# Performance work log

Hardware: AMD Instinct MI355X
Metric: run time of the kernel (lower is better)

The kernel has to match this reference:

```python
import jax, jax.numpy as jnp
import numpy as np

B, L, H, W, C = 2, 5, 48, 176, 256
HEADS, DIM_HEAD = 8, 32
INNER = HEADS * DIM_HEAD  # 256
SCALE = DIM_HEAD ** -0.5


def setup_inputs() -> dict:
    key = jax.random.key(0)
    k1, k2, k3, k4, k5 = jax.random.split(key, 5)
    x = jax.random.normal(k1, (B, L, H, W, C), dtype=jnp.float32)
    # mask of shape (B, H, W, 1, L); slot 0 always valid so no softmax row is fully masked
    mask = jax.random.randint(k2, (B, H, W, 1, L), 0, 2, dtype=jnp.int32)
    mask = mask.at[..., 0].set(1)
    w_qkv = jax.random.normal(k3, (C, 3 * INNER), dtype=jnp.float32) / np.sqrt(C)
    w_out = jax.random.normal(k4, (INNER, C), dtype=jnp.float32) / np.sqrt(INNER)
    b_out = jax.random.normal(k5, (C,), dtype=jnp.float32) * 0.01
    return {"x": x, "mask": mask, "w_qkv": w_qkv, "w_out": w_out, "b_out": b_out}


def reference(x, mask, w_qkv, w_out, b_out):
    # x: (B, L, H, W, C) -> (B, H, W, L, C)
    xp = jnp.transpose(x, (0, 2, 3, 1, 4))
    qkv = xp @ w_qkv  # (B, H, W, L, 3*INNER)
    q, k, v = jnp.split(qkv, 3, axis=-1)
    # split heads: (B, H, W, L, M, D)
    shp = (B, H, W, L, HEADS, DIM_HEAD)
    q = q.reshape(shp)
    k = k.reshape(shp)
    v = v.reshape(shp)
    # attention over the small CAV axis L
    att = jnp.einsum('bhwimd,bhwjmd->bmhwij', q, k) * SCALE  # (B,M,H,W,L,L)
    m = mask[:, None]  # (B,1,H,W,1,L) broadcasts over (B,M,H,W,i,j)
    att = jnp.where(m == 0, -jnp.inf, att)
    att = jax.nn.softmax(att, axis=-1)
    out = jnp.einsum('bmhwij,bhwjmd->bhwimd', att, v)  # (B,H,W,L,M,D)
    out = out.reshape(B, H, W, L, INNER)
    out = out @ w_out + b_out  # dropout is identity in eval
    return jnp.transpose(out, (0, 3, 1, 2, 4))  # (B, L, H, W, C)
```

## Files before the change

kernel.cpp:

```cpp
#include <hip/hip_runtime.h>


typedef __attribute__((ext_vector_type(8))) short short8;
typedef __attribute__((ext_vector_type(4))) float f32x4;

#define SCALE_F 0.17677669529663687f

static __device__ __forceinline__ float b2f(unsigned short u) {
    union { unsigned u; float f; } x; x.u = ((unsigned)u) << 16; return x.f;
}
static __device__ __forceinline__ unsigned short f2b(float f) {
    union { float f; unsigned u; } x; x.f = f;
    unsigned u = x.u;
    return (unsigned short)((u + 0x7FFFu + ((u >> 16) & 1u)) >> 16);
}

static __device__ __forceinline__ size_t row_to_xoff(int r) {
    int l = r % 5; int t = r / 5;
    int w = t % 176; t /= 176;
    int h = t % 48; int b = t / 48;
    return (size_t)(((b * 5 + l) * 48 + h) * 176 + w) * 256;
}

static __device__ __forceinline__ int lidx(int r, int c) {
    return r * 256 + ((((c >> 3) ^ (r & 7)) << 3) | (c & 7));
}

static __device__ __forceinline__ void barrier_lgkm() {
    __builtin_amdgcn_s_waitcnt(0xC07F);
    __builtin_amdgcn_s_barrier();
}

__global__ __launch_bounds__(256) void k_prep(const float* __restrict__ wq,
                                              const float* __restrict__ wo,
                                              unsigned short* __restrict__ wqt,
                                              unsigned short* __restrict__ wot) {
    __shared__ unsigned short tile[64 * 65];
    const int bb = blockIdx.x;
    const float* src; unsigned short* dst; int kt, nt, ncols;
    if (bb < 48) { kt = bb / 12; nt = bb % 12; src = wq; dst = wqt; ncols = 768; }
    else { int b2 = bb - 48; kt = b2 >> 2; nt = b2 & 3; src = wo; dst = wot; ncols = 256; }
    const int t = threadIdx.x;
#pragma unroll
    for (int p = 0; p < 4; ++p) {
        int u = p * 256 + t; int r = u >> 4, c4 = u & 15;
        float4 v = *(const float4*)&src[(size_t)(kt * 64 + r) * ncols + nt * 64 + c4 * 4];
        tile[r * 65 + c4 * 4 + 0] = f2b(v.x);
        tile[r * 65 + c4 * 4 + 1] = f2b(v.y);
        tile[r * 65 + c4 * 4 + 2] = f2b(v.z);
        tile[r * 65 + c4 * 4 + 3] = f2b(v.w);
    }
    __syncthreads();
#pragma unroll
    for (int p = 0; p < 2; ++p) {
        int u = p * 256 + t; int n = u >> 3, c8 = u & 7;
        short8 o;
#pragma unroll
        for (int j = 0; j < 8; ++j) o[j] = (short)tile[(c8 * 8 + j) * 65 + n];
        *(short8*)&dst[(nt * 64 + n) * 256 + kt * 64 + c8 * 8] = o;
    }
}

static __device__ __forceinline__ void cstore(const f32x4 (&acc)[5][2],
        unsigned short* __restrict__ Ds, int n0w, int lane) {
    const int ln = lane & 15, quad = lane >> 4;
#pragma unroll
    for (int m = 0; m < 5; ++m)
#pragma unroll
        for (int n = 0; n < 2; ++n)
#pragma unroll
            for (int rg = 0; rg < 4; ++rg)
                Ds[lidx(m * 16 + quad * 4 + rg, n0w + n * 16 + ln)] = f2b(acc[m][n][rg]);
}

__global__ __launch_bounds__(512, 2) void k_fused(const float* __restrict__ x,
                                                  const int* __restrict__ mask,
                                                  const unsigned short* __restrict__ wqt,
                                                  const unsigned short* __restrict__ wot,
                                                  const float* __restrict__ bo,
                                                  float* __restrict__ out) {
    __shared__ __align__(16) unsigned short xs[80 * 256];
    __shared__ __align__(16) unsigned short qs[80 * 256];
    __shared__ __align__(16) unsigned short kvs[80 * 256];

    const int tid = threadIdx.x;
    const int blk = blockIdx.x;
    const int rbase = blk * 80;
    const int lane = tid & 63, wv = tid >> 6;
    const int n0w = wv * 32;
    const int ln = lane & 15, quad = lane >> 4;

#pragma unroll
    for (int i = 0; i < 5; ++i) {
        int u = i * 512 + tid;
        int r = u >> 5, cb = u & 31;
        size_t xo = row_to_xoff(rbase + r) + cb * 8;
        float4 v0 = *(const float4*)(x + xo);
        float4 v1 = *(const float4*)(x + xo + 4);
        short8 o;
        o[0] = (short)f2b(v0.x); o[1] = (short)f2b(v0.y);
        o[2] = (short)f2b(v0.z); o[3] = (short)f2b(v0.w);
        o[4] = (short)f2b(v1.x); o[5] = (short)f2b(v1.y);
        o[6] = (short)f2b(v1.z); o[7] = (short)f2b(v1.w);
        *(short8*)&xs[lidx(r, cb * 8)] = o;
    }

    const int part = tid & 3, hh = (tid >> 2) & 7, g = tid >> 5;
    int mk[5];
#pragma unroll
    for (int j = 0; j < 5; ++j) mk[j] = mask[(blk * 16 + g) * 5 + j];

    const unsigned short* wq_l = wqt + (n0w + ln) * 256 + quad * 8;
    const unsigned short* wo_l = wot + (n0w + ln) * 256 + quad * 8;

    barrier_lgkm();

    f32x4 aq[5][2], ak[5][2], av[5][2];
#pragma unroll
    for (int m = 0; m < 5; ++m)
#pragma unroll
        for (int n = 0; n < 2; ++n) {
            aq[m][n] = (f32x4){0.f, 0.f, 0.f, 0.f};
            ak[m][n] = (f32x4){0.f, 0.f, 0.f, 0.f};
            av[m][n] = (f32x4){0.f, 0.f, 0.f, 0.f};
        }
#pragma unroll
    for (int kk = 0; kk < 8; ++kk) {
        short8 a[5];
#pragma unroll
        for (int m = 0; m < 5; ++m)
            a[m] = *(const short8*)&xs[lidx(m * 16 + ln, kk * 32 + quad * 8)];
        short8 bq[2], bk[2], bv[2];
#pragma unroll
        for (int n = 0; n < 2; ++n) {
            int o = n * (16 * 256) + kk * 32;
            bq[n] = *(const short8*)&wq_l[o];
            bk[n] = *(const short8*)&wq_l[o + 256 * 256];
            bv[n] = *(const short8*)&wq_l[o + 512 * 256];
        }
#pragma unroll
        for (int m = 0; m < 5; ++m)
#pragma unroll
            for (int n = 0; n < 2; ++n)
                aq[m][n] = __builtin_amdgcn_mfma_f32_16x16x32_bf16(a[m], bq[n], aq[m][n], 0, 0, 0);
#pragma unroll
        for (int m = 0; m < 5; ++m)
#pragma unroll
            for (int n = 0; n < 2; ++n)
                ak[m][n] = __builtin_amdgcn_mfma_f32_16x16x32_bf16(a[m], bk[n], ak[m][n], 0, 0, 0);
#pragma unroll
        for (int m = 0; m < 5; ++m)
#pragma unroll
            for (int n = 0; n < 2; ++n)
                av[m][n] = __builtin_amdgcn_mfma_f32_16x16x32_bf16(a[m], bv[n], av[m][n], 0, 0, 0);
    }
    cstore(aq, qs, n0w, lane);
    cstore(ak, kvs, n0w, lane);
    barrier_lgkm();

    float pr[5][5];
    {
        const int c0 = hh * 32 + part * 8;
        float qf[5][8];
#pragma unroll
        for (int i = 0; i < 5; ++i) {
            short8 qv = *(const short8*)&qs[lidx(g * 5 + i, c0)];
#pragma unroll
            for (int d = 0; d < 8; ++d) qf[i][d] = b2f((unsigned short)qv[d]);
        }
        float s[5][5];
#pragma unroll
        for (int j = 0; j < 5; ++j) {
            short8 kv = *(const short8*)&kvs[lidx(g * 5 + j, c0)];
            float kf[8];
#pragma unroll
            for (int d = 0; d < 8; ++d) kf[d] = b2f((unsigned short)kv[d]);
#pragma unroll
            for (int i = 0; i < 5; ++i) {
                float acc = 0.f;
#pragma unroll
                for (int d = 0; d < 8; ++d) acc += qf[i][d] * kf[d];
                s[i][j] = acc;
            }
        }
#pragma unroll
        for (int i = 0; i < 5; ++i)
#pragma unroll
            for (int j = 0; j < 5; ++j) {
                s[i][j] += __shfl_xor(s[i][j], 1, 64);
                s[i][j] += __shfl_xor(s[i][j], 2, 64);
            }
#pragma unroll
        for (int i = 0; i < 5; ++i) {
            float mx = -1e30f;
#pragma unroll
            for (int j = 0; j < 5; ++j) {
                s[i][j] = mk[j] ? s[i][j] * SCALE_F : -1e30f;
                mx = fmaxf(mx, s[i][j]);
            }
            float sum = 0.f;
#pragma unroll
            for (int j = 0; j < 5; ++j) { pr[i][j] = __expf(s[i][j] - mx); sum += pr[i][j]; }
            float inv = 1.f / sum;
#pragma unroll
            for (int j = 0; j < 5; ++j) pr[i][j] *= inv;
        }
    }
    barrier_lgkm();

    cstore(av, kvs, n0w, lane);
    barrier_lgkm();

    {
        const int c0 = hh * 32 + part * 8;
        float o[5][8];
#pragma unroll
        for (int i = 0; i < 5; ++i)
#pragma unroll
            for (int d = 0; d < 8; ++d) o[i][d] = 0.f;
#pragma unroll
        for (int j = 0; j < 5; ++j) {
            short8 vv = *(const short8*)&kvs[lidx(g * 5 + j, c0)];
            float vf[8];
#pragma unroll
            for (int d = 0; d < 8; ++d) vf[d] = b2f((unsigned short)vv[d]);
#pragma unroll
            for (int i = 0; i < 5; ++i)
#pragma unroll
                for (int d = 0; d < 8; ++d) o[i][d] += pr[i][j] * vf[d];
        }
#pragma unroll
        for (int i = 0; i < 5; ++i) {
            short8 ov;
#pragma unroll
            for (int d = 0; d < 8; ++d) ov[d] = (short)f2b(o[i][d]);
            *(short8*)&kvs[lidx(g * 5 + i, c0)] = ov;
        }
    }
    barrier_lgkm();

    {
        f32x4 ao[5][2];
#pragma unroll
        for (int m = 0; m < 5; ++m)
#pragma unroll
            for (int n = 0; n < 2; ++n) ao[m][n] = (f32x4){0.f, 0.f, 0.f, 0.f};
#pragma unroll
        for (int kk = 0; kk < 8; ++kk) {
            short8 a[5];
#pragma unroll
            for (int m = 0; m < 5; ++m)
                a[m] = *(const short8*)&kvs[lidx(m * 16 + ln, kk * 32 + quad * 8)];
            short8 bn[2];
#pragma unroll
            for (int n = 0; n < 2; ++n)
                bn[n] = *(const short8*)&wo_l[n * (16 * 256) + kk * 32];
#pragma unroll
            for (int m = 0; m < 5; ++m)
#pragma unroll
                for (int n = 0; n < 2; ++n)
                    ao[m][n] = __builtin_amdgcn_mfma_f32_16x16x32_bf16(a[m], bn[n], ao[m][n], 0, 0, 0);
        }
        float bv2[2];
#pragma unroll
        for (int n = 0; n < 2; ++n) bv2[n] = bo[n0w + n * 16 + ln];
#pragma unroll
        for (int m = 0; m < 5; ++m)
#pragma unroll
            for (int rg = 0; rg < 4; ++rg) {
                int row = m * 16 + quad * 4 + rg;
                size_t off = row_to_xoff(rbase + row);
#pragma unroll
                for (int n = 0; n < 2; ++n)
                    out[off + n0w + n * 16 + ln] = ao[m][n][rg] + bv2[n];
            }
    }
}

extern "C" void kernel_launch(void* const* d_in, const int* in_sizes, int n_in,
                              void* d_out, int out_size, void* d_ws, size_t ws_size,
                              hipStream_t stream) {
    const float* x   = (const float*)d_in[0];
    const int* mask  = (const int*)d_in[1];
    const float* wq  = (const float*)d_in[2];
    const float* wo  = (const float*)d_in[3];
    const float* bo  = (const float*)d_in[4];
    float* out = (float*)d_out;

    char* ws = (char*)d_ws;
    unsigned short* wqt = (unsigned short*)(ws);
    unsigned short* wot = (unsigned short*)(ws + 393216);

    hipLaunchKernelGGL(k_prep, dim3(64), dim3(256), 0, stream, wq, wo, wqt, wot);
    hipLaunchKernelGGL(k_fused, dim3(1056), dim3(512), 0, stream, x, mask, wqt, wot, bo, out);
}
```

Before: 267.8 us.

## Double block to 1024 threads with 16 output columns per wave

The fused block now launches 1024 threads (16 waves), and each wave computes one 16-column MFMA tile instead of two, which halves the accumulator register footprint per thread. The V projection is moved into a separate loop that overlaps with the Q/K stores, and only the first 512 threads run the scalar attention stage. This is meant to raise latency hiding and wave occupancy, but half the threads sit idle during attention. Barriers also now span 16 waves, and launch bounds of 1024 with 4 blocks per CU may force register spills.

New measurement: 273.5 us. +2.1%, slower.

```diff
diff --git a/kernel.cpp b/kernel.cpp
--- a/kernel.cpp
+++ b/kernel.cpp
@@ -61,24 +61,22 @@
     }
 }
 
-static __device__ __forceinline__ void cstore(const f32x4 (&acc)[5][2],
+static __device__ __forceinline__ void cstore1(const f32x4 (&acc)[5],
         unsigned short* __restrict__ Ds, int n0w, int lane) {
     const int ln = lane & 15, quad = lane >> 4;
 #pragma unroll
     for (int m = 0; m < 5; ++m)
 #pragma unroll
-        for (int n = 0; n < 2; ++n)
-#pragma unroll
-            for (int rg = 0; rg < 4; ++rg)
-                Ds[lidx(m * 16 + quad * 4 + rg, n0w + n * 16 + ln)] = f2b(acc[m][n][rg]);
-}
-
-__global__ __launch_bounds__(512, 2) void k_fused(const float* __restrict__ x,
-                                                  const int* __restrict__ mask,
-                                                  const unsigned short* __restrict__ wqt,
-                                                  const unsigned short* __restrict__ wot,
-                                                  const float* __restrict__ bo,
-                                                  float* __restrict__ out) {
+        for (int rg = 0; rg < 4; ++rg)
+            Ds[lidx(m * 16 + quad * 4 + rg, n0w + ln)] = f2b(acc[m][rg]);
+}
+
+__global__ __launch_bounds__(1024, 4) void k_fused(const float* __restrict__ x,
+                                                   const int* __restrict__ mask,
+                                                   const unsigned short* __restrict__ wqt,
+                                                   const unsigned short* __restrict__ wot,
+                                                   const float* __restrict__ bo,
+                                                   float* __restrict__ out) {
     __shared__ __align__(16) unsigned short xs[80 * 256];
     __shared__ __align__(16) unsigned short qs[80 * 256];
     __shared__ __align__(16) unsigned short kvs[80 * 256];
@@ -87,79 +85,80 @@
     const int blk = blockIdx.x;
     const int rbase = blk * 80;
     const int lane = tid & 63, wv = tid >> 6;
-    const int n0w = wv * 32;
+    const int n0w = wv * 16;
     const int ln = lane & 15, quad = lane >> 4;
 
 #pragma unroll
-    for (int i = 0; i < 5; ++i) {
-        int u = i * 512 + tid;
-        int r = u >> 5, cb = u & 31;
-        size_t xo = row_to_xoff(rbase + r) + cb * 8;
-        float4 v0 = *(const float4*)(x + xo);
-        float4 v1 = *(const float4*)(x + xo + 4);
-        short8 o;
-        o[0] = (short)f2b(v0.x); o[1] = (short)f2b(v0.y);
-        o[2] = (short)f2b(v0.z); o[3] = (short)f2b(v0.w);
-        o[4] = (short)f2b(v1.x); o[5] = (short)f2b(v1.y);
-        o[6] = (short)f2b(v1.z); o[7] = (short)f2b(v1.w);
-        *(short8*)&xs[lidx(r, cb * 8)] = o;
-    }
-
-    const int part = tid & 3, hh = (tid >> 2) & 7, g = tid >> 5;
+    for (int i = 0; i < 3; ++i) {
+        int u = i * 1024 + tid;
+        if (u < 2560) {
+            int r = u >> 5, cb = u & 31;
+            size_t xo = row_to_xoff(rbase + r) + cb * 8;
+            float4 v0 = *(const float4*)(x + xo);
+            float4 v1 = *(const float4*)(x + xo + 4);
+            short8 o;
+            o[0] = (short)f2b(v0.x); o[1] = (short)f2b(v0.y);
+            o[2] = (short)f2b(v0.z); o[3] = (short)f2b(v0.w);
+            o[4] = (short)f2b(v1.x); o[5] = (short)f2b(v1.y);
+            o[6] = (short)f2b(v1.z); o[7] = (short)f2b(v1.w);
+            *(short8*)&xs[lidx(r, cb * 8)] = o;
+        }
+    }
+
+    const bool act = tid < 512;
+    const int part = tid & 3, hh = (tid >> 2) & 7, g = (tid >> 5) & 15;
     int mk[5];
 #pragma unroll
-    for (int j = 0; j < 5; ++j) mk[j] = mask[(blk * 16 + g) * 5 + j];
+    for (int j = 0; j < 5; ++j) mk[j] = act ? mask[(blk * 16 + g) * 5 + j] : 1;
 
     const unsigned short* wq_l = wqt + (n0w + ln) * 256 + quad * 8;
     const unsigned short* wo_l = wot + (n0w + ln) * 256 + quad * 8;
 
     barrier_lgkm();
 
-    f32x4 aq[5][2], ak[5][2], av[5][2];
-#pragma unroll
-    for (int m = 0; m < 5; ++m)
-#pragma unroll
-        for (int n = 0; n < 2; ++n) {
-            aq[m][n] = (f32x4){0.f, 0.f, 0.f, 0.f};
-            ak[m][n] = (f32x4){0.f, 0.f, 0.f, 0.f};
-            av[m][n] = (f32x4){0.f, 0.f, 0.f, 0.f};
-        }
+    f32x4 aq[5], ak[5];
+#pragma unroll
+    for (int m = 0; m < 5; ++m) {
+        aq[m] = (f32x4){0.f, 0.f, 0.f, 0.f};
+        ak[m] = (f32x4){0.f, 0.f, 0.f, 0.f};
+    }
 #pragma unroll
     for (int kk = 0; kk < 8; ++kk) {
         short8 a[5];
 #pragma unroll
         for (int m = 0; m < 5; ++m)
             a[m] = *(const short8*)&xs[lidx(m * 16 + ln, kk * 32 + quad * 8)];
-        short8 bq[2], bk[2], bv[2];
-#pragma unroll
-        for (int n = 0; n < 2; ++n) {
-            int o = n * (16 * 256) + kk * 32;
-            bq[n] = *(const short8*)&wq_l[o];
-            bk[n] = *(const short8*)&wq_l[o + 256 * 256];
-            bv[n] = *(const short8*)&wq_l[o + 512 * 256];
-        }
-#pragma unroll
-        for (int m = 0; m < 5; ++m)
-#pragma unroll
-            for (int n = 0; n < 2; ++n)
-                aq[m][n] = __builtin_amdgcn_mfma_f32_16x16x32_bf16(a[m], bq[n], aq[m][n], 0, 0, 0);
-#pragma unroll
-        for (int m = 0; m < 5; ++m)
-#pragma unroll
-            for (int n = 0; n < 2; ++n)
-                ak[m][n] = __builtin_amdgcn_mfma_f32_16x16x32_bf16(a[m], bk[n], ak[m][n], 0, 0, 0);
-#pragma unroll
-        for (int m = 0; m < 5; ++m)
-#pragma unroll
-            for (int n = 0; n < 2; ++n)
-                av[m][n] = __builtin_amdgcn_mfma_f32_16x16x32_bf16(a[m], bv[n], av[m][n], 0, 0, 0);
-    }
-    cstore(aq, qs, n0w, lane);
-    cstore(ak, kvs, n0w, lane);
+        short8 bq = *(const short8*)&wq_l[kk * 32];
+        short8 bk = *(const short8*)&wq_l[65536 + kk * 32];
+#pragma unroll
+        for (int m = 0; m < 5; ++m)
+            aq[m] = __builtin_amdgcn_mfma_f32_16x16x32_bf16(a[m], bq, aq[m], 0, 0, 0);
+#pragma unroll
+        for (int m = 0; m < 5; ++m)
+            ak[m] = __builtin_amdgcn_mfma_f32_16x16x32_bf16(a[m], bk, ak[m], 0, 0, 0);
+    }
+    cstore1(aq, qs, n0w, lane);
+    cstore1(ak, kvs, n0w, lane);
+
+    f32x4 av[5];
+#pragma unroll
+    for (int m = 0; m < 5; ++m) av[m] = (f32x4){0.f, 0.f, 0.f, 0.f};
+#pragma unroll
+    for (int kk = 0; kk < 8; ++kk) {
+        short8 a[5];
+#pragma unroll
+        for (int m = 0; m < 5; ++m)
+            a[m] = *(const short8*)&xs[lidx(m * 16 + ln, kk * 32 + quad * 8)];
+        short8 bv = *(const short8*)&wq_l[131072 + kk * 32];
+#pragma unroll
+        for (int m = 0; m < 5; ++m)
+            av[m] = __builtin_amdgcn_mfma_f32_16x16x32_bf16(a[m], bv, av[m], 0, 0, 0);
+    }
+
     barrier_lgkm();
 
     float pr[5][5];
-    {
+    if (act) {
         const int c0 = hh * 32 + part * 8;
         float qf[5][8];
 #pragma unroll
@@ -208,10 +207,10 @@
     }
     barrier_lgkm();
 
-    cstore(av, kvs, n0w, lane);
-    barrier_lgkm();
-
-    {
+    cstore1(av, kvs, n0w, lane);
+    barrier_lgkm();
+
+    if (act) {
         const int c0 = hh * 32 + part * 8;
         float o[5][8];
 #pragma unroll
@@ -240,39 +239,28 @@
     barrier_lgkm();
 
     {
-        f32x4 ao[5][2];
-#pragma unroll
-        for (int m = 0; m < 5; ++m)
-#pragma unroll
-            for (int n = 0; n < 2; ++n) ao[m][n] = (f32x4){0.f, 0.f, 0.f, 0.f};
+        f32x4 ao[5];
+#pragma unroll
+        for (int m = 0; m < 5; ++m) ao[m] = (f32x4){0.f, 0.f, 0.f, 0.f};
 #pragma unroll
         for (int kk = 0; kk < 8; ++kk) {
             short8 a[5];
 #pragma unroll
             for (int m = 0; m < 5; ++m)
                 a[m] = *(const short8*)&kvs[lidx(m * 16 + ln, kk * 32 + quad * 8)];
-            short8 bn[2];
-#pragma unroll
-            for (int n = 0; n < 2; ++n)
-                bn[n] = *(const short8*)&wo_l[n * (16 * 256) + kk * 32];
+            short8 bn = *(const short8*)&wo_l[kk * 32];
 #pragma unroll
             for (int m = 0; m < 5; ++m)
-#pragma unroll
-                for (int n = 0; n < 2; ++n)
-                    ao[m][n] = __builtin_amdgcn_mfma_f32_16x16x32_bf16(a[m], bn[n], ao[m][n], 0, 0, 0);
-        }
-        float bv2[2];
-#pragma unroll
-        for (int n = 0; n < 2; ++n) bv2[n] = bo[n0w + n * 16 + ln];
+                ao[m] = __builtin_amdgcn_mfma_f32_16x16x32_bf16(a[m], bn, ao[m], 0, 0, 0);
+        }
+        float bv2 = bo[n0w + ln];
 #pragma unroll
         for (int m = 0; m < 5; ++m)
 #pragma unroll
             for (int rg = 0; rg < 4; ++rg) {
                 int row = m * 16 + quad * 4 + rg;
                 size_t off = row_to_xoff(rbase + row);
-#pragma unroll
-                for (int n = 0; n < 2; ++n)
-                    out[off + n0w + n * 16 + ln] = ao[m][n][rg] + bv2[n];
+                out[off + n0w + ln] = ao[m][rg] + bv2;
             }
     }
 }
@@ -292,5 +280,5 @@
     unsigned short* wot = (unsigned short*)(ws + 393216);
 
     hipLaunchKernelGGL(k_prep, dim3(64), dim3(256), 0, stream, wq, wo, wqt, wot);
-    hipLaunchKernelGGL(k_fused, dim3(1056), dim3(512), 0, stream, x, mask, wqt, wot, bo, out);
-}
+    hipLaunchKernelGGL(k_fused, dim3(1056), dim3(1024), 0, stream, x, mask, wqt, wot, bo, out);
+}
```

## Halve rows per block and split V projection to raise occupancy

Applied to the files above, without the earlier changes.

Each block now handles 40 rows (8 pixel groups) instead of 80, with shared buffers shrunk to 48 rows and the grid doubled to 2112 blocks. The V projection runs as a separate pass after Q/K are stored, which cuts the live accumulator count, and launch bounds ask for 4 blocks per CU. The aim is higher occupancy and better latency hiding. The cost is wasted MFMA work on padded rows 40-47, idle threads in the attention phase (only 256 of 512 active), and the x tile being read from LDS twice.

Measured after the change: 297.8 us. +11.2%, slower.

```diff
diff --git a/kernel.cpp b/kernel.cpp
--- a/kernel.cpp
+++ b/kernel.cpp
@@ -61,11 +61,11 @@
     }
 }
 
-static __device__ __forceinline__ void cstore(const f32x4 (&acc)[5][2],
+static __device__ __forceinline__ void cstore(const f32x4 (&acc)[3][2],
         unsigned short* __restrict__ Ds, int n0w, int lane) {
     const int ln = lane & 15, quad = lane >> 4;
 #pragma unroll
-    for (int m = 0; m < 5; ++m)
+    for (int m = 0; m < 3; ++m)
 #pragma unroll
         for (int n = 0; n < 2; ++n)
 #pragma unroll
@@ -73,93 +73,111 @@
                 Ds[lidx(m * 16 + quad * 4 + rg, n0w + n * 16 + ln)] = f2b(acc[m][n][rg]);
 }
 
-__global__ __launch_bounds__(512, 2) void k_fused(const float* __restrict__ x,
+__global__ __launch_bounds__(512, 4) void k_fused(const float* __restrict__ x,
                                                   const int* __restrict__ mask,
                                                   const unsigned short* __restrict__ wqt,
                                                   const unsigned short* __restrict__ wot,
                                                   const float* __restrict__ bo,
                                                   float* __restrict__ out) {
-    __shared__ __align__(16) unsigned short xs[80 * 256];
-    __shared__ __align__(16) unsigned short qs[80 * 256];
-    __shared__ __align__(16) unsigned short kvs[80 * 256];
+    __shared__ __align__(16) unsigned short xs[48 * 256];
+    __shared__ __align__(16) unsigned short qs[48 * 256];
+    __shared__ __align__(16) unsigned short kvs[48 * 256];
 
     const int tid = threadIdx.x;
     const int blk = blockIdx.x;
-    const int rbase = blk * 80;
+    const int rbase = blk * 40;
     const int lane = tid & 63, wv = tid >> 6;
     const int n0w = wv * 32;
     const int ln = lane & 15, quad = lane >> 4;
 
 #pragma unroll
-    for (int i = 0; i < 5; ++i) {
+    for (int i = 0; i < 3; ++i) {
         int u = i * 512 + tid;
-        int r = u >> 5, cb = u & 31;
-        size_t xo = row_to_xoff(rbase + r) + cb * 8;
-        float4 v0 = *(const float4*)(x + xo);
-        float4 v1 = *(const float4*)(x + xo + 4);
-        short8 o;
-        o[0] = (short)f2b(v0.x); o[1] = (short)f2b(v0.y);
-        o[2] = (short)f2b(v0.z); o[3] = (short)f2b(v0.w);
-        o[4] = (short)f2b(v1.x); o[5] = (short)f2b(v1.y);
-        o[6] = (short)f2b(v1.z); o[7] = (short)f2b(v1.w);
-        *(short8*)&xs[lidx(r, cb * 8)] = o;
-    }
-
-    const int part = tid & 3, hh = (tid >> 2) & 7, g = tid >> 5;
+        if (u < 1280) {
+            int r = u >> 5, cb = u & 31;
+            size_t xo = row_to_xoff(rbase + r) + cb * 8;
+            float4 v0 = *(const float4*)(x + xo);
+            float4 v1 = *(const float4*)(x + xo + 4);
+            short8 o;
+            o[0] = (short)f2b(v0.x); o[1] = (short)f2b(v0.y);
+            o[2] = (short)f2b(v0.z); o[3] = (short)f2b(v0.w);
+            o[4] = (short)f2b(v1.x); o[5] = (short)f2b(v1.y);
+            o[6] = (short)f2b(v1.z); o[7] = (short)f2b(v1.w);
+            *(short8*)&xs[lidx(r, cb * 8)] = o;
+        }
+    }
+
+    const bool act = tid < 256;
+    const int part = tid & 3, hh = (tid >> 2) & 7, g = (tid >> 5) & 7;
     int mk[5];
 #pragma unroll
-    for (int j = 0; j < 5; ++j) mk[j] = mask[(blk * 16 + g) * 5 + j];
+    for (int j = 0; j < 5; ++j) mk[j] = act ? mask[(blk * 8 + g) * 5 + j] : 1;
 
     const unsigned short* wq_l = wqt + (n0w + ln) * 256 + quad * 8;
     const unsigned short* wo_l = wot + (n0w + ln) * 256 + quad * 8;
 
     barrier_lgkm();
 
-    f32x4 aq[5][2], ak[5][2], av[5][2];
-#pragma unroll
-    for (int m = 0; m < 5; ++m)
+    f32x4 aq[3][2], ak[3][2];
+#pragma unroll
+    for (int m = 0; m < 3; ++m)
 #pragma unroll
         for (int n = 0; n < 2; ++n) {
             aq[m][n] = (f32x4){0.f, 0.f, 0.f, 0.f};
             ak[m][n] = (f32x4){0.f, 0.f, 0.f, 0.f};
-            av[m][n] = (f32x4){0.f, 0.f, 0.f, 0.f};
         }
 #pragma unroll
     for (int kk = 0; kk < 8; ++kk) {
-        short8 a[5];
-#pragma unroll
-        for (int m = 0; m < 5; ++m)
+        short8 a[3];
+#pragma unroll
+        for (int m = 0; m < 3; ++m)
             a[m] = *(const short8*)&xs[lidx(m * 16 + ln, kk * 32 + quad * 8)];
-        short8 bq[2], bk[2], bv[2];
+        short8 bq[2], bk[2];
 #pragma unroll
         for (int n = 0; n < 2; ++n) {
-            int o = n * (16 * 256) + kk * 32;
-            bq[n] = *(const short8*)&wq_l[o];
-            bk[n] = *(const short8*)&wq_l[o + 256 * 256];
-            bv[n] = *(const short8*)&wq_l[o + 512 * 256];
-        }
-#pragma unroll
-        for (int m = 0; m < 5; ++m)
+            bq[n] = *(const short8*)&wq_l[n * 4096 + kk * 32];
+            bk[n] = *(const short8*)&wq_l[65536 + n * 4096 + kk * 32];
+        }
+#pragma unroll
+        for (int m = 0; m < 3; ++m)
 #pragma unroll
             for (int n = 0; n < 2; ++n)
                 aq[m][n] = __builtin_amdgcn_mfma_f32_16x16x32_bf16(a[m], bq[n], aq[m][n], 0, 0, 0);
 #pragma unroll
-        for (int m = 0; m < 5; ++m)
+        for (int m = 0; m < 3; ++m)
 #pragma unroll
             for (int n = 0; n < 2; ++n)
                 ak[m][n] = __builtin_amdgcn_mfma_f32_16x16x32_bf16(a[m], bk[n], ak[m][n], 0, 0, 0);
-#pragma unroll
-        for (int m = 0; m < 5; ++m)
+    }
+    cstore(aq, qs, n0w, lane);
+    cstore(ak, kvs, n0w, lane);
+
+    f32x4 av[3][2];
+#pragma unroll
+    for (int m = 0; m < 3; ++m)
+#pragma unroll
+        for (int n = 0; n < 2; ++n) av[m][n] = (f32x4){0.f, 0.f, 0.f, 0.f};
+#pragma unroll
+    for (int kk = 0; kk < 8; ++kk) {
+        short8 a[3];
+#pragma unroll
+        for (int m = 0; m < 3; ++m)
+            a[m] = *(const short8*)&xs[lidx(m * 16 + ln, kk * 32 + quad * 8)];
+        short8 bv[2];
+#pragma unroll
+        for (int n = 0; n < 2; ++n)
+            bv[n] = *(const short8*)&wq_l[131072 + n * 4096 + kk * 32];
+#pragma unroll
+        for (int m = 0; m < 3; ++m)
 #pragma unroll
             for (int n = 0; n < 2; ++n)
                 av[m][n] = __builtin_amdgcn_mfma_f32_16x16x32_bf16(a[m], bv[n], av[m][n], 0, 0, 0);
     }
-    cstore(aq, qs, n0w, lane);
-    cstore(ak, kvs, n0w, lane);
+
     barrier_lgkm();
 
     float pr[5][5];
-    {
+    if (act) {
         const int c0 = hh * 32 + part * 8;
         float qf[5][8];
 #pragma unroll
@@ -211,7 +229,7 @@
     cstore(av, kvs, n0w, lane);
     barrier_lgkm();
 
-    {
+    if (act) {
         const int c0 = hh * 32 + part * 8;
         float o[5][8];
 #pragma unroll
@@ -240,23 +258,23 @@
     barrier_lgkm();
 
     {
-        f32x4 ao[5][2];
-#pragma unroll
-        for (int m = 0; m < 5; ++m)
+        f32x4 ao[3][2];
+#pragma unroll
+        for (int m = 0; m < 3; ++m)
 #pragma unroll
             for (int n = 0; n < 2; ++n) ao[m][n] = (f32x4){0.f, 0.f, 0.f, 0.f};
 #pragma unroll
         for (int kk = 0; kk < 8; ++kk) {
-            short8 a[5];
-#pragma unroll
-            for (int m = 0; m < 5; ++m)
+            short8 a[3];
+#pragma unroll
+            for (int m = 0; m < 3; ++m)
                 a[m] = *(const short8*)&kvs[lidx(m * 16 + ln, kk * 32 + quad * 8)];
             short8 bn[2];
 #pragma unroll
             for (int n = 0; n < 2; ++n)
-                bn[n] = *(const short8*)&wo_l[n * (16 * 256) + kk * 32];
-#pragma unroll
-            for (int m = 0; m < 5; ++m)
+                bn[n] = *(const short8*)&wo_l[n * 4096 + kk * 32];
+#pragma unroll
+            for (int m = 0; m < 3; ++m)
 #pragma unroll
                 for (int n = 0; n < 2; ++n)
                     ao[m][n] = __builtin_amdgcn_mfma_f32_16x16x32_bf16(a[m], bn[n], ao[m][n], 0, 0, 0);
@@ -265,14 +283,16 @@
 #pragma unroll
         for (int n = 0; n < 2; ++n) bv2[n] = bo[n0w + n * 16 + ln];
 #pragma unroll
-        for (int m = 0; m < 5; ++m)
+        for (int m = 0; m < 3; ++m)
 #pragma unroll
             for (int rg = 0; rg < 4; ++rg) {
                 int row = m * 16 + quad * 4 + rg;
-                size_t off = row_to_xoff(rbase + row);
-#pragma unroll
-                for (int n = 0; n < 2; ++n)
-                    out[off + n0w + n * 16 + ln] = ao[m][n][rg] + bv2[n];
+                if (row < 40) {
+                    size_t off = row_to_xoff(rbase + row);
+#pragma unroll
+                    for (int n = 0; n < 2; ++n)
+                        out[off + n0w + n * 16 + ln] = ao[m][n][rg] + bv2[n];
+                }
             }
     }
 }
@@ -292,5 +312,5 @@
     unsigned short* wot = (unsigned short*)(ws + 393216);
 
     hipLaunchKernelGGL(k_prep, dim3(64), dim3(256), 0, stream, wq, wo, wqt, wot);
-    hipLaunchKernelGGL(k_fused, dim3(1056), dim3(512), 0, stream, x, mask, wqt, wot, bo, out);
-}
+    hipLaunchKernelGGL(k_fused, dim3(2112), dim3(512), 0, stream, x, mask, wqt, wot, bo, out);
+}
```

## Stream weight chunks into LDS with async global_load_lds double buffering

Applied to the files above, without the earlier changes.

Weight tiles for the QKV and output projections are now copied straight from global memory into a per-wave double-buffered LDS region using global_load_lds, with the next chunk issued two steps ahead and vmcnt waits placed by hand. Before, the MFMA loop read its weight fragments directly from global memory. The goal is to hide global latency behind the MFMAs. The change also replaces scalar bf16 rounding with packed v_cvt_pk_bf16_f32 conversions. This adds 32KB of LDS per block, which may limit how many blocks fit per CU, and relies on fragile hand-coded waitcnt immediates.

New measurement: 239.2 us. 10.7% less time.

```diff
diff --git a/kernel.cpp b/kernel.cpp
--- a/kernel.cpp
+++ b/kernel.cpp
@@ -13,6 +13,11 @@
     union { float f; unsigned u; } x; x.f = f;
     unsigned u = x.u;
     return (unsigned short)((u + 0x7FFFu + ((u >> 16) & 1u)) >> 16);
+}
+static __device__ __forceinline__ unsigned pk_bf16(float lo, float hi) {
+    unsigned u;
+    asm("v_cvt_pk_bf16_f32 %0, %1, %2" : "=v"(u) : "v"(lo), "v"(hi));
+    return u;
 }
 
 static __device__ __forceinline__ size_t row_to_xoff(int r) {
@@ -24,6 +29,12 @@
 
 static __device__ __forceinline__ int lidx(int r, int c) {
     return r * 256 + ((((c >> 3) ^ (r & 7)) << 3) | (c & 7));
+}
+
+static __device__ __forceinline__ void async_cp16(const unsigned short* g, unsigned short* l) {
+    __builtin_amdgcn_global_load_lds(
+        (__attribute__((address_space(1))) void*)(void*)g,
+        (__attribute__((address_space(3))) void*)(void*)l, 16, 0, 0);
 }
 
 static __device__ __forceinline__ void barrier_lgkm() {
@@ -61,16 +72,98 @@
     }
 }
 
+template<int C>
+static __device__ __forceinline__ void issue_chunk(const unsigned short* __restrict__ wqt,
+                                                   const unsigned short* __restrict__ wot,
+                                                   unsigned short* __restrict__ Bw,
+                                                   int n0w, int lane) {
+    constexpr int sel = (C < 24) ? (C % 3) : 3;
+    constexpr int kk  = (C < 24) ? (C / 3) : (C - 24);
+    constexpr int slot = C & 1;
+    const unsigned short* wbase = (sel < 3) ? (wqt + sel * 65536) : wot;
+#pragma unroll
+    for (int t = 0; t < 2; ++t) {
+        int cidx = t * 64 + lane;
+        int nl = cidx >> 2;
+        int kq = (cidx & 3) ^ ((nl >> 1) & 3);
+        const unsigned short* g = wbase + (n0w + nl) * 256 + kk * 32 + kq * 8;
+        async_cp16(g, Bw + slot * 1024 + t * 512);
+    }
+}
+
+#define MFMA_ALL(ACC)                                                               \
+    _Pragma("unroll")                                                               \
+    for (int m = 0; m < 5; ++m)                                                     \
+        _Pragma("unroll")                                                           \
+        for (int n = 0; n < 2; ++n)                                                 \
+            ACC[m][n] = __builtin_amdgcn_mfma_f32_16x16x32_bf16(a[m], b[n], ACC[m][n], 0, 0, 0);
+
+template<int C>
+static __device__ __forceinline__ void qkv_step(f32x4 (&aq)[5][2], f32x4 (&ak)[5][2],
+        f32x4 (&av)[5][2], short8 (&a)[5],
+        const unsigned short* __restrict__ As, unsigned short* __restrict__ Bw,
+        const unsigned short* __restrict__ wqt, const unsigned short* __restrict__ wot,
+        int n0w, int lane) {
+    constexpr int sel = C % 3;
+    constexpr int kk = C / 3;
+    constexpr int slot = C & 1;
+    const int ln = lane & 15, quad = lane >> 4;
+    __builtin_amdgcn_s_waitcnt(0xF72);
+    short8 b[2];
+#pragma unroll
+    for (int n = 0; n < 2; ++n)
+        b[n] = *(const short8*)&Bw[slot * 1024 + (n * 16 + ln) * 32
+                                   + ((quad ^ ((ln >> 1) & 3)) * 8)];
+    __builtin_amdgcn_s_waitcnt(0xC07F);
+    if constexpr (C + 2 < 32) issue_chunk<C + 2>(wqt, wot, Bw, n0w, lane);
+    if constexpr (sel == 0) {
+#pragma unroll
+        for (int m = 0; m < 5; ++m)
+            a[m] = *(const short8*)&As[lidx(m * 16 + ln, kk * 32 + quad * 8)];
+    }
+    if constexpr (sel == 0) { MFMA_ALL(aq) } else if constexpr (sel == 1) { MFMA_ALL(ak) }
+    else { MFMA_ALL(av) }
+}
+
+template<int C>
+static __device__ __forceinline__ void out_step(f32x4 (&ao)[5][2],
+        const unsigned short* __restrict__ As, unsigned short* __restrict__ Bw,
+        const unsigned short* __restrict__ wqt, const unsigned short* __restrict__ wot,
+        int n0w, int lane) {
+    constexpr int kk = C - 24;
+    constexpr int slot = C & 1;
+    constexpr int imm = (C == 31) ? 0xF70 : 0xF72;
+    const int ln = lane & 15, quad = lane >> 4;
+    __builtin_amdgcn_s_waitcnt(imm);
+    short8 b[2];
+#pragma unroll
+    for (int n = 0; n < 2; ++n)
+        b[n] = *(const short8*)&Bw[slot * 1024 + (n * 16 + ln) * 32
+                                   + ((quad ^ ((ln >> 1) & 3)) * 8)];
+    __builtin_amdgcn_s_waitcnt(0xC07F);
+    if constexpr (C + 2 < 32) issue_chunk<C + 2>(wqt, wot, Bw, n0w, lane);
+    short8 a[5];
+#pragma unroll
+    for (int m = 0; m < 5; ++m)
+        a[m] = *(const short8*)&As[lidx(m * 16 + ln, kk * 32 + quad * 8)];
+    MFMA_ALL(ao)
+}
+
 static __device__ __forceinline__ void cstore(const f32x4 (&acc)[5][2],
         unsigned short* __restrict__ Ds, int n0w, int lane) {
     const int ln = lane & 15, quad = lane >> 4;
 #pragma unroll
     for (int m = 0; m < 5; ++m)
 #pragma unroll
-        for (int n = 0; n < 2; ++n)
-#pragma unroll
-            for (int rg = 0; rg < 4; ++rg)
-                Ds[lidx(m * 16 + quad * 4 + rg, n0w + n * 16 + ln)] = f2b(acc[m][n][rg]);
+        for (int n = 0; n < 2; ++n) {
+            const int col = n0w + n * 16 + ln, r0 = m * 16 + quad * 4;
+            unsigned p01 = pk_bf16(acc[m][n][0], acc[m][n][1]);
+            unsigned p23 = pk_bf16(acc[m][n][2], acc[m][n][3]);
+            Ds[lidx(r0 + 0, col)] = (unsigned short)p01;
+            Ds[lidx(r0 + 1, col)] = (unsigned short)(p01 >> 16);
+            Ds[lidx(r0 + 2, col)] = (unsigned short)p23;
+            Ds[lidx(r0 + 3, col)] = (unsigned short)(p23 >> 16);
+        }
 }
 
 __global__ __launch_bounds__(512, 2) void k_fused(const float* __restrict__ x,
@@ -82,6 +175,7 @@
     __shared__ __align__(16) unsigned short xs[80 * 256];
     __shared__ __align__(16) unsigned short qs[80 * 256];
     __shared__ __align__(16) unsigned short kvs[80 * 256];
+    __shared__ __align__(16) unsigned short Bb[8 * 2048];
 
     const int tid = threadIdx.x;
     const int blk = blockIdx.x;
@@ -89,6 +183,7 @@
     const int lane = tid & 63, wv = tid >> 6;
     const int n0w = wv * 32;
     const int ln = lane & 15, quad = lane >> 4;
+    unsigned short* Bw = Bb + wv * 2048;
 
 #pragma unroll
     for (int i = 0; i < 5; ++i) {
@@ -97,12 +192,12 @@
         size_t xo = row_to_xoff(rbase + r) + cb * 8;
         float4 v0 = *(const float4*)(x + xo);
         float4 v1 = *(const float4*)(x + xo + 4);
-        short8 o;
-        o[0] = (short)f2b(v0.x); o[1] = (short)f2b(v0.y);
-        o[2] = (short)f2b(v0.z); o[3] = (short)f2b(v0.w);
-        o[4] = (short)f2b(v1.x); o[5] = (short)f2b(v1.y);
-        o[6] = (short)f2b(v1.z); o[7] = (short)f2b(v1.w);
-        *(short8*)&xs[lidx(r, cb * 8)] = o;
+        int4 o;
+        o.x = (int)pk_bf16(v0.x, v0.y);
+        o.y = (int)pk_bf16(v0.z, v0.w);
+        o.z = (int)pk_bf16(v1.x, v1.y);
+        o.w = (int)pk_bf16(v1.z, v1.w);
+        *(int4*)&xs[lidx(r, cb * 8)] = o;
     }
 
     const int part = tid & 3, hh = (tid >> 2) & 7, g = tid >> 5;
@@ -110,8 +205,8 @@
 #pragma unroll
     for (int j = 0; j < 5; ++j) mk[j] = mask[(blk * 16 + g) * 5 + j];
 
-    const unsigned short* wq_l = wqt + (n0w + ln) * 256 + quad * 8;
-    const unsigned short* wo_l = wot + (n0w + ln) * 256 + quad * 8;
+    issue_chunk<0>(wqt, wot, Bw, n0w, lane);
+    issue_chunk<1>(wqt, wot, Bw, n0w, lane);
 
     barrier_lgkm();
 
@@ -124,35 +219,32 @@
             ak[m][n] = (f32x4){0.f, 0.f, 0.f, 0.f};
             av[m][n] = (f32x4){0.f, 0.f, 0.f, 0.f};
         }
-#pragma unroll
-    for (int kk = 0; kk < 8; ++kk) {
+    {
         short8 a[5];
-#pragma unroll
-        for (int m = 0; m < 5; ++m)
-            a[m] = *(const short8*)&xs[lidx(m * 16 + ln, kk * 32 + quad * 8)];
-        short8 bq[2], bk[2], bv[2];
-#pragma unroll
-        for (int n = 0; n < 2; ++n) {
-            int o = n * (16 * 256) + kk * 32;
-            bq[n] = *(const short8*)&wq_l[o];
-            bk[n] = *(const short8*)&wq_l[o + 256 * 256];
-            bv[n] = *(const short8*)&wq_l[o + 512 * 256];
-        }
-#pragma unroll
-        for (int m = 0; m < 5; ++m)
-#pragma unroll
-            for (int n = 0; n < 2; ++n)
-                aq[m][n] = __builtin_amdgcn_mfma_f32_16x16x32_bf16(a[m], bq[n], aq[m][n], 0, 0, 0);
-#pragma unroll
-        for (int m = 0; m < 5; ++m)
-#pragma unroll
-            for (int n = 0; n < 2; ++n)
-                ak[m][n] = __builtin_amdgcn_mfma_f32_16x16x32_bf16(a[m], bk[n], ak[m][n], 0, 0, 0);
-#pragma unroll
-        for (int m = 0; m < 5; ++m)
-#pragma unroll
-            for (int n = 0; n < 2; ++n)
-                av[m][n] = __builtin_amdgcn_mfma_f32_16x16x32_bf16(a[m], bv[n], av[m][n], 0, 0, 0);
+        qkv_step<0>(aq, ak, av, a, xs, Bw, wqt, wot, n0w, lane);
+        qkv_step<1>(aq, ak, av, a, xs, Bw, wqt, wot, n0w, lane);
+        qkv_step<2>(aq, ak, av, a, xs, Bw, wqt, wot, n0w, lane);
+        qkv_step<3>(aq, ak, av, a, xs, Bw, wqt, wot, n0w, lane);
+        qkv_step<4>(aq, ak, av, a, xs, Bw, wqt, wot, n0w, lane);
+        qkv_step<5>(aq, ak, av, a, xs, Bw, wqt, wot, n0w, lane);
+        qkv_step<6>(aq, ak, av, a, xs, Bw, wqt, wot, n0w, lane);
+        qkv_step<7>(aq, ak, av, a, xs, Bw, wqt, wot, n0w, lane);
+        qkv_step<8>(aq, ak, av, a, xs, Bw, wqt, wot, n0w, lane);
+        qkv_step<9>(aq, ak, av, a, xs, Bw, wqt, wot, n0w, lane);
+        qkv_step<10>(aq, ak, av, a, xs, Bw, wqt, wot, n0w, lane);
+        qkv_step<11>(aq, ak, av, a, xs, Bw, wqt, wot, n0w, lane);
+        qkv_step<12>(aq, ak, av, a, xs, Bw, wqt, wot, n0w, lane);
+        qkv_step<13>(aq, ak, av, a, xs, Bw, wqt, wot, n0w, lane);
+        qkv_step<14>(aq, ak, av, a, xs, Bw, wqt, wot, n0w, lane);
+        qkv_step<15>(aq, ak, av, a, xs, Bw, wqt, wot, n0w, lane);
+        qkv_step<16>(aq, ak, av, a, xs, Bw, wqt, wot, n0w, lane);
+        qkv_step<17>(aq, ak, av, a, xs, Bw, wqt, wot, n0w, lane);
+        qkv_step<18>(aq, ak, av, a, xs, Bw, wqt, wot, n0w, lane);
+        qkv_step<19>(aq, ak, av, a, xs, Bw, wqt, wot, n0w, lane);
+        qkv_step<20>(aq, ak, av, a, xs, Bw, wqt, wot, n0w, lane);
+        qkv_step<21>(aq, ak, av, a, xs, Bw, wqt, wot, n0w, lane);
+        qkv_step<22>(aq, ak, av, a, xs, Bw, wqt, wot, n0w, lane);
+        qkv_step<23>(aq, ak, av, a, xs, Bw, wqt, wot, n0w, lane);
     }
     cstore(aq, qs, n0w, lane);
     cstore(ak, kvs, n0w, lane);
@@ -231,10 +323,12 @@
         }
 #pragma unroll
         for (int i = 0; i < 5; ++i) {
-            short8 ov;
-#pragma unroll
-            for (int d = 0; d < 8; ++d) ov[d] = (short)f2b(o[i][d]);
-            *(short8*)&kvs[lidx(g * 5 + i, c0)] = ov;
+            int4 ov;
+            ov.x = (int)pk_bf16(o[i][0], o[i][1]);
+            ov.y = (int)pk_bf16(o[i][2], o[i][3]);
+            ov.z = (int)pk_bf16(o[i][4], o[i][5]);
+            ov.w = (int)pk_bf16(o[i][6], o[i][7]);
+            *(int4*)&kvs[lidx(g * 5 + i, c0)] = ov;
         }
     }
     barrier_lgkm();
@@ -245,22 +339,14 @@
         for (int m = 0; m < 5; ++m)
 #pragma unroll
             for (int n = 0; n < 2; ++n) ao[m][n] = (f32x4){0.f, 0.f, 0.f, 0.f};
-#pragma unroll
-        for (int kk = 0; kk < 8; ++kk) {
-            short8 a[5];
-#pragma unroll
-            for (int m = 0; m < 5; ++m)
-                a[m] = *(const short8*)&kvs[lidx(m * 16 + ln, kk * 32 + quad * 8)];
-            short8 bn[2];
-#pragma unroll
-            for (int n = 0; n < 2; ++n)
-                bn[n] = *(const short8*)&wo_l[n * (16 * 256) + kk * 32];
-#pragma unroll
-            for (int m = 0; m < 5; ++m)
-#pragma unroll
-                for (int n = 0; n < 2; ++n)
-                    ao[m][n] = __builtin_amdgcn_mfma_f32_16x16x32_bf16(a[m], bn[n], ao[m][n], 0, 0, 0);
-        }
+        out_step<24>(ao, kvs, Bw, wqt, wot, n0w, lane);
+        out_step<25>(ao, kvs, Bw, wqt, wot, n0w, lane);
+        out_step<26>(ao, kvs, Bw, wqt, wot, n0w, lane);
+        out_step<27>(ao, kvs, Bw, wqt, wot, n0w, lane);
+        out_step<28>(ao, kvs, Bw, wqt, wot, n0w, lane);
+        out_step<29>(ao, kvs, Bw, wqt, wot, n0w, lane);
+        out_step<30>(ao, kvs, Bw, wqt, wot, n0w, lane);
+        out_step<31>(ao, kvs, Bw, wqt, wot, n0w, lane);
         float bv2[2];
 #pragma unroll
         for (int n = 0; n < 2; ++n) bv2[n] = bo[n0w + n * 16 + ln];
```
